# Optimization experiments

Measured on AMD Instinct MI355X. Metric: run time of the kernel, lower is better.

The kernel has to match this reference:

```python
import jax, jax.numpy as jnp
import numpy as np

N_NODES = 50000


def gcn_conv(x, W, b, src, dst):
    # PyG GCNConv: h = x @ W; add self-loops; norm = deg^{-1/2}[src]*deg^{-1/2}[dst];
    # out = scatter_add(norm * h[src] -> dst) + bias
    h = x @ W  # [N, out]
    ones = jnp.ones(src.shape[0], dtype=x.dtype)
    deg = jax.ops.segment_sum(ones, dst, num_segments=N_NODES) + 1.0  # +1 for self-loop
    inv_sqrt = deg ** -0.5
    norm = inv_sqrt[src] * inv_sqrt[dst]  # [E]
    msgs = h[src] * norm[:, None]  # [E, out]
    agg = jax.ops.segment_sum(msgs, dst, num_segments=N_NODES)
    # self-loop contribution: norm_ii = deg_i^{-1}
    agg = agg + h * (inv_sqrt * inv_sqrt)[:, None]
    return agg + b


def setup_inputs() -> dict:
    key = jax.random.key(0)
    k1, k2, k3, k4 = jax.random.split(key, 4)
    d_in, d_h = 256, 256
    x = jax.random.normal(k1, (N_NODES, d_in), dtype=jnp.float32)
    edge_index = jax.random.randint(k2, (2, 800000), 0, N_NODES, dtype=jnp.int64)
    # Glorot-style params (GCNConv linear has no bias; separate bias added post-agg)
    W1 = jax.random.normal(k3, (d_in, d_h), dtype=jnp.float32) / np.sqrt(d_in)
    W2 = jax.random.normal(k4, (d_h, d_h), dtype=jnp.float32) / np.sqrt(d_h)
    b1 = jnp.zeros((d_h,), dtype=jnp.float32)
    b2 = jnp.zeros((d_h,), dtype=jnp.float32)
    return {"x": x, "edge_index": edge_index, "W1": W1, "b1": b1, "W2": W2, "b2": b2}


def reference(x, edge_index, W1, b1, W2, b2):
    src, dst = edge_index[0], edge_index[1]
    h = jax.nn.relu(gcn_conv(x, W1, b1, src, dst))
    h = jax.nn.relu(gcn_conv(h, W2, b2, src, dst))
    # global_mean_pool with batch=arange(N) assigns each node its own graph -> identity
    return h
```

## Files before the change

### kernel.cpp

```cpp
#include <hip/hip_runtime.h>
#include <hip/hip_bf16.h>

typedef unsigned short u16;
typedef unsigned int u32;

#define N_NODES 50000
#define N_EDGES 800000
#define DHID 256
#define ELLW 64

typedef __attribute__((ext_vector_type(8))) _Float16 f16x8;
typedef __attribute__((ext_vector_type(4))) float f32x4;
typedef __attribute__((ext_vector_type(2))) float f32x2;

__device__ __forceinline__ u16 f2bf(float f) {
    u32 u = __float_as_uint(f);
    u32 r = (u + 0x7FFFu + ((u >> 16) & 1u)) >> 16;
    return (u16)r;
}
__device__ __forceinline__ u16 f2h(float f) {
    _Float16 h = (_Float16)f;
    union { _Float16 h; u16 u; } c; c.h = h;
    return c.u;
}
__device__ __forceinline__ void gl_lds16(const void* g, void* l) {
    __builtin_amdgcn_global_load_lds(
        (const __attribute__((address_space(1))) u32*)g,
        (__attribute__((address_space(3))) u32*)l, 16, 0, 0);
}

#define ZW_BLKS 196
#define W_BLKS 512
#define SPLIT_BLKS 12500
__global__ void prep_all(const float* __restrict__ x, u16* __restrict__ xf,
                         const float* __restrict__ W1, const float* __restrict__ W2,
                         u16* __restrict__ W1t, u16* __restrict__ W2t,
                         int* __restrict__ deg, u32* __restrict__ hs32) {
    const int b = blockIdx.x, tid = threadIdx.x;
    if (b < ZW_BLKS) {
        int j = b * 256 + tid;
        if (j < N_NODES) deg[j] = 0;
        if (j < 128) hs32[(size_t)N_NODES * 128 + j] = 0;
    } else if (b < ZW_BLKS + W_BLKS) {
        int idx = b - ZW_BLKS;
        int y = idx >> 8, n = idx & 255, k = tid;
        const float* W = y ? W2 : W1;
        u16* o = y ? W2t : W1t;
        o[n * 256 + k] = f2h(W[k * 256 + n]);
    } else {
        int i = (b - ZW_BLKS - W_BLKS) * 256 + tid;
        float4 v = ((const float4*)x)[i];
        uint2 hv;
        hv.x = (u32)f2h(v.x) | ((u32)f2h(v.y) << 16);
        hv.y = (u32)f2h(v.z) | ((u32)f2h(v.w) << 16);
        ((uint2*)xf)[i] = hv;
    }
}

#define FILL_BLKS 1563
__global__ void fill_kernel(const int* __restrict__ src, const int* __restrict__ dst,
                            int* __restrict__ deg, u16* __restrict__ col16) {
    const int tid = threadIdx.x;
    const int e0 = blockIdx.x * 512 + tid;
    const int e1 = e0 + 256;
    const bool ok0 = (e0 < N_EDGES), ok1 = (e1 < N_EDGES);
    int d0, d1, s0, s1, p0, p1;
    if (ok0) { d0 = dst[e0]; s0 = src[e0]; }
    if (ok1) { d1 = dst[e1]; s1 = src[e1]; }
    if (ok0) p0 = atomicAdd(&deg[d0], 1);
    if (ok1) p1 = atomicAdd(&deg[d1], 1);
    if (ok0 && p0 < ELLW) col16[(size_t)d0 * ELLW + p0] = (u16)s0;
    if (ok1 && p1 < ELLW) col16[(size_t)d1 * ELLW + p1] = (u16)s1;
}

__global__ __launch_bounds__(256) void gemm_f16_kernel(
    const u16* __restrict__ Af, const u16* __restrict__ Bt,
    const int* __restrict__ deg, u16* __restrict__ out, int M) {
    __shared__ u16 As[128 * 32];
    __shared__ u16 Bs[128 * 32];
    const int tid = threadIdx.x;
    const int wave = tid >> 6;
    const int lane = tid & 63;
    const int wm = wave >> 1, wn = wave & 1;
    const int quad = lane >> 4, l16 = lane & 15;
    const int m0 = blockIdx.x * 128;
    const int n0 = blockIdx.y * 128;

    f32x4 acc[4][4] = {};

    const int row0 = tid >> 2, row1 = (256 + tid) >> 2;
    const int kk = (tid & 3) * 8;
    int ar0 = m0 + row0; if (ar0 >= M) ar0 = M - 1;
    int ar1 = m0 + row1; if (ar1 >= M) ar1 = M - 1;
    const size_t aoff0 = (size_t)ar0 * 256 + kk;
    const size_t aoff1 = (size_t)ar1 * 256 + kk;
    const size_t boff0 = (size_t)(n0 + row0) * 256 + kk;
    const size_t boff1 = (size_t)(n0 + row1) * 256 + kk;
    const size_t l0 = (size_t)(wave * 64) * 8;
    const size_t l1 = (size_t)(256 + wave * 64) * 8;

    for (int ko = 0; ko < 8; ++ko) {
        const int koff = ko * 32;
        __syncthreads();
        gl_lds16(Af + aoff0 + koff, &As[l0]);
        gl_lds16(Af + aoff1 + koff, &As[l1]);
        gl_lds16(Bt + boff0 + koff, &Bs[l0]);
        gl_lds16(Bt + boff1 + koff, &Bs[l1]);
        asm volatile("s_waitcnt vmcnt(0)" ::: "memory");
        __syncthreads();

        f16x8 af[4], bf[4];
#pragma unroll
        for (int mi = 0; mi < 4; ++mi)
            af[mi] = *(const f16x8*)&As[(wm * 64 + mi * 16 + l16) * 32 + quad * 8];
#pragma unroll
        for (int ni = 0; ni < 4; ++ni)
            bf[ni] = *(const f16x8*)&Bs[(wn * 64 + ni * 16 + l16) * 32 + quad * 8];
#pragma unroll
        for (int mi = 0; mi < 4; ++mi)
#pragma unroll
            for (int ni = 0; ni < 4; ++ni)
                acc[mi][ni] = __builtin_amdgcn_mfma_f32_16x16x32_f16(af[mi], bf[ni], acc[mi][ni], 0, 0, 0);
    }

#pragma unroll
    for (int mi = 0; mi < 4; ++mi) {
#pragma unroll
        for (int r = 0; r < 4; ++r) {
            int row = m0 + wm * 64 + mi * 16 + quad * 4 + r;
            if (row < M) {
                float s = rsqrtf((float)deg[row] + 1.0f);
#pragma unroll
                for (int ni = 0; ni < 4; ++ni) {
                    int c = n0 + wn * 64 + ni * 16 + l16;
                    out[(size_t)row * 256 + c] = f2bf(acc[mi][ni][r] * s);
                }
            }
        }
    }
}

__global__ __launch_bounds__(256) void agg_kernel(
    const u16* __restrict__ hs, const u16* __restrict__ col16,
    const int* __restrict__ deg, const float* __restrict__ bias,
    u16* __restrict__ out_f16, float* __restrict__ out_f,
    int mode, int Nn) {
    const int wave = threadIdx.x >> 6, lane = threadIdx.x & 63;
    const int i = blockIdx.x * 4 + wave;
    if (i >= Nn) return;

    const int cnt = deg[i];
    const size_t ebase = (size_t)i * ELLW;
    int entry = Nn;
    if (lane == 0) entry = i;
    else if (lane - 1 < cnt) entry = (int)col16[ebase + lane - 1];
    int entries = cnt + 1;
    if (entries > 64) entries = 64;
    const int nb = (entries + 3) >> 2;
    const size_t lofs = (size_t)lane * 4;

    f32x2 a01 = {0.f, 0.f}, a23 = {0.f, 0.f};

#define ISSUE(b, x0, x1, x2, x3)                                                \
    {                                                                           \
        int e0 = __builtin_amdgcn_readlane(entry, (b) * 4 + 0);                 \
        int e1 = __builtin_amdgcn_readlane(entry, (b) * 4 + 1);                 \
        int e2 = __builtin_amdgcn_readlane(entry, (b) * 4 + 2);                 \
        int e3 = __builtin_amdgcn_readlane(entry, (b) * 4 + 3);                 \
        x0 = *(const uint2*)(hs + (size_t)e0 * 256 + lofs);                     \
        x1 = *(const uint2*)(hs + (size_t)e1 * 256 + lofs);                     \
        x2 = *(const uint2*)(hs + (size_t)e2 * 256 + lofs);                     \
        x3 = *(const uint2*)(hs + (size_t)e3 * 256 + lofs);                     \
    }
#define ACCUM(v)                                                                \
    {                                                                           \
        f32x2 p0, p1;                                                           \
        p0.x = __uint_as_float(v.x << 16);                                      \
        p0.y = __uint_as_float(v.x & 0xffff0000u);                              \
        p1.x = __uint_as_float(v.y << 16);                                      \
        p1.y = __uint_as_float(v.y & 0xffff0000u);                              \
        a01 += p0; a23 += p1;                                                   \
    }

    uint2 c0, c1, c2, c3, d0, d1, d2, d3, n0v, n1v, n2v, n3v;
    ISSUE(0, c0, c1, c2, c3);
    if (nb > 1) ISSUE(1, d0, d1, d2, d3);
    for (int b = 0; b < nb; ++b) {
        const bool more2 = (b + 2 < nb);
        if (more2) ISSUE(b + 2, n0v, n1v, n2v, n3v);
        ACCUM(c0); ACCUM(c1); ACCUM(c2); ACCUM(c3);
        c0 = d0; c1 = d1; c2 = d2; c3 = d3;
        d0 = n0v; d1 = n1v; d2 = n2v; d3 = n3v;
    }
    {
        int cap = cnt < ELLW ? cnt : ELLW;
        for (int j = 63; j < cap; ++j) {
            int s = (int)col16[ebase + j];
            uint2 v = *(const uint2*)(hs + (size_t)s * 256 + lofs);
            ACCUM(v);
        }
    }
#undef ISSUE
#undef ACCUM

    const float inv = rsqrtf((float)cnt + 1.0f);
    float4 bb = *(const float4*)(bias + lane * 4);
    float r0 = fmaxf(fmaf(a01.x, inv, bb.x), 0.0f);
    float r1 = fmaxf(fmaf(a01.y, inv, bb.y), 0.0f);
    float r2 = fmaxf(fmaf(a23.x, inv, bb.z), 0.0f);
    float r3 = fmaxf(fmaf(a23.y, inv, bb.w), 0.0f);
    const size_t o = (size_t)i * 256 + lane * 4;
    if (mode == 0) {
        u16 h0 = f2h(r0), h1 = f2h(r1), h2 = f2h(r2), h3 = f2h(r3);
        uint2 w;
        w.x = (u32)h0 | ((u32)h1 << 16);
        w.y = (u32)h2 | ((u32)h3 << 16);
        *(uint2*)(out_f16 + o) = w;
    } else {
        *(float4*)(out_f + o) = make_float4(r0, r1, r2, r3);
    }
}

extern "C" void kernel_launch(void* const* d_in, const int* in_sizes, int n_in,
                              void* d_out, int out_size, void* d_ws, size_t ws_size,
                              hipStream_t stream) {
    const float* x = (const float*)d_in[0];
    const int* ei = (const int*)d_in[1];
    const float* W1 = (const float*)d_in[2];
    const float* b1 = (const float*)d_in[3];
    const float* W2 = (const float*)d_in[4];
    const float* b2 = (const float*)d_in[5];
    float* out = (float*)d_out;

    const int Nn = N_NODES, E = N_EDGES;
    const int* srcp = ei;
    const int* dstp = ei + E;

    char* p = (char*)d_ws;
    auto take = [&](size_t bytes) -> void* {
        void* r = (void*)p;
        p += (bytes + 255) & ~(size_t)255;
        return r;
    };
    u16* hs    = (u16*)take((size_t)(Nn + 1) * DHID * 2);
    u16* col16 = (u16*)take((size_t)Nn * ELLW * 2);
    int* deg   = (int*)take((size_t)Nn * 4);
    u16* W1t   = (u16*)take(256 * 256 * 2);
    u16* W2t   = (u16*)take(256 * 256 * 2);
    size_t used = (size_t)(p - (char*)d_ws);
    size_t af_bytes = (size_t)Nn * DHID * 2;
    u16* Af = (ws_size >= used + af_bytes) ? (u16*)take(af_bytes) : (u16*)d_out;

    prep_all<<<ZW_BLKS + W_BLKS + SPLIT_BLKS, 256, 0, stream>>>(
        x, Af, W1, W2, W1t, W2t, deg, (u32*)hs);
    fill_kernel<<<FILL_BLKS, 256, 0, stream>>>(srcp, dstp, deg, col16);

    const int gm = (Nn + 127) / 128;
    gemm_f16_kernel<<<dim3(gm, 2), 256, 0, stream>>>(Af, W1t, deg, hs, Nn);
    agg_kernel<<<(Nn + 3) / 4, 256, 0, stream>>>(hs, col16, deg, b1, Af, nullptr, 0, Nn);
    gemm_f16_kernel<<<dim3(gm, 2), 256, 0, stream>>>(Af, W2t, deg, hs, Nn);
    agg_kernel<<<(Nn + 3) / 4, 256, 0, stream>>>(hs, col16, deg, b2, nullptr, out, 1, Nn);
}
```

Baseline: 317.7 us.

## Widen GEMM tile to full output width and batch more edges per fill thread

Each GEMM block now computes all 256 output columns, so an A tile is loaded once instead of once per column half. This takes 4x8 MFMA accumulators per wave, which raises register pressure. The ELL fill kernel now handles 8 edges per thread instead of 2, so more atomics are in flight per thread and fewer blocks are launched. The first GEMM is launched with a z dimension of 2 that the kernel never reads, so two blocks per row tile compute and write the same output.

```diff
diff --git a/kernel.cpp b/kernel.cpp
--- a/kernel.cpp
+++ b/kernel.cpp
@@ -57,36 +57,40 @@
     }
 }
 
-#define FILL_BLKS 1563
+#define FILL_BLKS 391
 __global__ void fill_kernel(const int* __restrict__ src, const int* __restrict__ dst,
                             int* __restrict__ deg, u16* __restrict__ col16) {
     const int tid = threadIdx.x;
-    const int e0 = blockIdx.x * 512 + tid;
-    const int e1 = e0 + 256;
-    const bool ok0 = (e0 < N_EDGES), ok1 = (e1 < N_EDGES);
-    int d0, d1, s0, s1, p0, p1;
-    if (ok0) { d0 = dst[e0]; s0 = src[e0]; }
-    if (ok1) { d1 = dst[e1]; s1 = src[e1]; }
-    if (ok0) p0 = atomicAdd(&deg[d0], 1);
-    if (ok1) p1 = atomicAdd(&deg[d1], 1);
-    if (ok0 && p0 < ELLW) col16[(size_t)d0 * ELLW + p0] = (u16)s0;
-    if (ok1 && p1 < ELLW) col16[(size_t)d1 * ELLW + p1] = (u16)s1;
-}
-
-__global__ __launch_bounds__(256) void gemm_f16_kernel(
+    const int e0 = blockIdx.x * 2048 + tid;
+    int ds[8], ps[8], ss[8];
+    bool ok[8];
+#pragma unroll
+    for (int q = 0; q < 8; ++q) {
+        int e = e0 + q * 256;
+        ok[q] = (e < N_EDGES);
+        if (ok[q]) { ds[q] = dst[e]; ss[q] = src[e]; }
+    }
+#pragma unroll
+    for (int q = 0; q < 8; ++q)
+        if (ok[q]) ps[q] = atomicAdd(&deg[ds[q]], 1);
+#pragma unroll
+    for (int q = 0; q < 8; ++q)
+        if (ok[q] && ps[q] < ELLW) col16[(size_t)ds[q] * ELLW + ps[q]] = (u16)ss[q];
+}
+
+__global__ __launch_bounds__(256) void gemm_sn_kernel(
     const u16* __restrict__ Af, const u16* __restrict__ Bt,
     const int* __restrict__ deg, u16* __restrict__ out, int M) {
     __shared__ u16 As[128 * 32];
-    __shared__ u16 Bs[128 * 32];
+    __shared__ u16 Bs[256 * 32];
     const int tid = threadIdx.x;
     const int wave = tid >> 6;
     const int lane = tid & 63;
     const int wm = wave >> 1, wn = wave & 1;
     const int quad = lane >> 4, l16 = lane & 15;
     const int m0 = blockIdx.x * 128;
-    const int n0 = blockIdx.y * 128;
-
-    f32x4 acc[4][4] = {};
+
+    f32x4 acc[4][8] = {};
 
     const int row0 = tid >> 2, row1 = (256 + tid) >> 2;
     const int kk = (tid & 3) * 8;
@@ -94,32 +98,35 @@
     int ar1 = m0 + row1; if (ar1 >= M) ar1 = M - 1;
     const size_t aoff0 = (size_t)ar0 * 256 + kk;
     const size_t aoff1 = (size_t)ar1 * 256 + kk;
-    const size_t boff0 = (size_t)(n0 + row0) * 256 + kk;
-    const size_t boff1 = (size_t)(n0 + row1) * 256 + kk;
-    const size_t l0 = (size_t)(wave * 64) * 8;
-    const size_t l1 = (size_t)(256 + wave * 64) * 8;
+    size_t boff[4];
+#pragma unroll
+    for (int c = 0; c < 4; ++c)
+        boff[c] = (size_t)(row0 + c * 64) * 256 + kk;
+    const size_t l0 = (size_t)wave * 512;
+    const size_t l1 = 2048 + (size_t)wave * 512;
 
     for (int ko = 0; ko < 8; ++ko) {
         const int koff = ko * 32;
         __syncthreads();
         gl_lds16(Af + aoff0 + koff, &As[l0]);
         gl_lds16(Af + aoff1 + koff, &As[l1]);
-        gl_lds16(Bt + boff0 + koff, &Bs[l0]);
-        gl_lds16(Bt + boff1 + koff, &Bs[l1]);
+#pragma unroll
+        for (int c = 0; c < 4; ++c)
+            gl_lds16(Bt + boff[c] + koff, &Bs[(size_t)c * 2048 + l0]);
         asm volatile("s_waitcnt vmcnt(0)" ::: "memory");
         __syncthreads();
 
-        f16x8 af[4], bf[4];
+        f16x8 af[4], bf[8];
 #pragma unroll
         for (int mi = 0; mi < 4; ++mi)
             af[mi] = *(const f16x8*)&As[(wm * 64 + mi * 16 + l16) * 32 + quad * 8];
 #pragma unroll
-        for (int ni = 0; ni < 4; ++ni)
-            bf[ni] = *(const f16x8*)&Bs[(wn * 64 + ni * 16 + l16) * 32 + quad * 8];
+        for (int ni = 0; ni < 8; ++ni)
+            bf[ni] = *(const f16x8*)&Bs[(wn * 128 + ni * 16 + l16) * 32 + quad * 8];
 #pragma unroll
         for (int mi = 0; mi < 4; ++mi)
 #pragma unroll
-            for (int ni = 0; ni < 4; ++ni)
+            for (int ni = 0; ni < 8; ++ni)
                 acc[mi][ni] = __builtin_amdgcn_mfma_f32_16x16x32_f16(af[mi], bf[ni], acc[mi][ni], 0, 0, 0);
     }
 
@@ -131,8 +138,8 @@
             if (row < M) {
                 float s = rsqrtf((float)deg[row] + 1.0f);
 #pragma unroll
-                for (int ni = 0; ni < 4; ++ni) {
-                    int c = n0 + wn * 64 + ni * 16 + l16;
+                for (int ni = 0; ni < 8; ++ni) {
+                    int c = wn * 128 + ni * 16 + l16;
                     out[(size_t)row * 256 + c] = f2bf(acc[mi][ni][r] * s);
                 }
             }
@@ -256,8 +263,8 @@
     fill_kernel<<<FILL_BLKS, 256, 0, stream>>>(srcp, dstp, deg, col16);
 
     const int gm = (Nn + 127) / 128;
-    gemm_f16_kernel<<<dim3(gm, 2), 256, 0, stream>>>(Af, W1t, deg, hs, Nn);
+    gemm_sn_kernel<<<dim3(gm, 1, 2), 256, 0, stream>>>(Af, W1t, deg, hs, Nn);
     agg_kernel<<<(Nn + 3) / 4, 256, 0, stream>>>(hs, col16, deg, b1, Af, nullptr, 0, Nn);
-    gemm_f16_kernel<<<dim3(gm, 2), 256, 0, stream>>>(Af, W2t, deg, hs, Nn);
+    gemm_sn_kernel<<<dim3(gm, 1, 1), 256, 0, stream>>>(Af, W2t, deg, hs, Nn);
     agg_kernel<<<(Nn + 3) / 4, 256, 0, stream>>>(hs, col16, deg, b2, nullptr, out, 1, Nn);
 }
```

Measured after the change: 350.7 us. +10.4%, slower.
